# Optimization experiments

Hardware: AMD Instinct MI355X
Metric: run time of the kernel (lower is better)

## Reference

```python
import jax, jax.numpy as jnp
import numpy as np

B, T, F_IN, F_OUT, N, TP, K = 32, 12, 16, 32, 2048, 12, 3
RED = 4  # SE reduction ratio


def _conv2d(x, w, b):
    # x: [b,c,h,w_] NCHW, w: [o,i,kh,kw] OIHW, VALID padding (matches nn.Conv2d default)
    y = jax.lax.conv_general_dilated(x, w, window_strides=(1, 1), padding='VALID',
                                     dimension_numbers=('NCHW', 'OIHW', 'NCHW'))
    return y + b[None, :, None, None]


def _tconv(x, w, b, tp):
    # Tconv1: conv (1,2) -> self-pad time axis back to tp with trailing slices -> relu
    y = _conv2d(x, w, b)
    t = y.shape[-1]
    if t < tp:
        y = jnp.concatenate([y[..., -(tp - t):], y], axis=-1)
    return jax.nn.relu(y)


def setup_inputs() -> dict:
    rng = np.random.default_rng(0)
    # symmetric nonneg adjacency
    W = rng.random((N, N), dtype=np.float32)
    W = (W + W.T) * 0.5
    D = np.diag(W.sum(axis=1))
    L = (D - W).astype(np.float32)
    # lambda_max via power iteration (replaces scipy eigs 'LR')
    v = rng.standard_normal(N).astype(np.float32)
    for _ in range(100):
        v = L @ v
        v /= np.linalg.norm(v)
    lam = float(v @ (L @ v))
    Lt = (2.0 * L / lam - np.eye(N, dtype=np.float32)).astype(np.float32)
    # NOTE: original code uses ELEMENTWISE '*' (numpy) in the Chebyshev recurrence; replicate faithfully
    cheb = [np.eye(N, dtype=np.float32), Lt.copy()]
    for _ in range(2, K):
        cheb.append(2.0 * Lt * cheb[-1] - cheb[-2])
    cheb = jnp.asarray(np.stack(cheb))  # [K, N, N]

    key = jax.random.key(0)
    ks = jax.random.split(key, 16)
    s = 0.05
    hid = T // RED
    return {
        'x': jax.random.normal(ks[0], (B, T, F_IN, N), dtype=jnp.float32),
        'cheb': cheb,
        'theta1': jax.random.normal(ks[1], (K, F_IN, F_OUT), dtype=jnp.float32) * s,
        'theta2': jax.random.normal(ks[2], (K, F_OUT, F_OUT), dtype=jnp.float32) * s,
        'mlp1_w': jax.random.normal(ks[3], (hid, T), dtype=jnp.float32) * s,
        'mlp1_b': jnp.zeros((hid,), dtype=jnp.float32),
        'mlp2_w': jax.random.normal(ks[4], (T, hid), dtype=jnp.float32) * s,
        'mlp2_b': jnp.zeros((T,), dtype=jnp.float32),
        'tc1_w': jax.random.normal(ks[5], (F_OUT, F_OUT, 1, 2), dtype=jnp.float32) * s,
        'tc1_b': jnp.zeros((F_OUT,), dtype=jnp.float32),
        'tc2_w': jax.random.normal(ks[6], (F_OUT, F_OUT, 1, 2), dtype=jnp.float32) * s,
        'tc2_b': jnp.zeros((F_OUT,), dtype=jnp.float32),
        'res_w': jax.random.normal(ks[7], (F_OUT, F_IN, 1, 1), dtype=jnp.float32) * s,
        'res_b': jnp.zeros((F_OUT,), dtype=jnp.float32),
        'ln_g': jnp.ones((N,), dtype=jnp.float32),
        'ln_b': jnp.zeros((N,), dtype=jnp.float32),
    }


def reference(x, cheb, theta1, theta2, mlp1_w, mlp1_b, mlp2_w, mlp2_b,
              tc1_w, tc1_b, tc2_w, tc2_b, res_w, res_b, ln_g, ln_b):
    # --- SE channel attention over the t axis ---
    att = x.mean(axis=(2, 3))                            # [b,t] (AvgPool over full (f,n))
    att = jax.nn.relu(att @ mlp1_w.T + mlp1_b)
    att = jax.nn.sigmoid(att @ mlp2_w.T + mlp2_b)
    x_att = x * att[:, :, None, None]                    # [b,t,f,n]

    # --- Chebyshev graph conv: fused over time t and order k ---
    def gconv(h, theta):
        # original: for t, for k: (h[b,:,f,t] @ T_k) then (@ theta_k), summed over k
        z = jnp.einsum('btfm,kmn->bktfn', h, cheb)       # graph mixing, [b,K,t,f,n]
        return jnp.einsum('bktfn,kfo->bton', z, theta)   # feature mixing + k-sum -> [b,t,o,n]

    xg = jax.nn.relu(gconv(x_att, theta1))
    xg = jax.nn.relu(gconv(xg, theta2))                  # [b,t,F_OUT,n]

    # --- temporal convs ---
    xt = _tconv(xg.transpose(0, 2, 3, 1), tc1_w, tc1_b, TP)   # [b,F_OUT,n,TP]
    xt = _tconv(xt, tc2_w, tc2_b, TP).transpose(0, 3, 1, 2)   # [b,TP,F_OUT,n]

    # --- residual 1x1 conv on the original input ---
    tshort = xg.shape[1] - xt.shape[1]                   # == 0 with t == tp
    x_res = _conv2d(x[:, tshort:].transpose(0, 2, 3, 1), res_w, res_b).transpose(0, 3, 1, 2)

    y = xt + x_res                                       # [b,TP,F_OUT,n]
    # LayerNorm over last (node) axis, eps=1e-5, biased variance (torch default)
    mu = y.mean(axis=-1, keepdims=True)
    var = ((y - mu) ** 2).mean(axis=-1, keepdims=True)
    y = (y - mu) / jnp.sqrt(var + 1e-5) * ln_g + ln_b
    return jax.nn.relu(y)
```

## Files before the change

### kernel.cpp

```cpp
#include <hip/hip_runtime.h>

#define DI __device__ __forceinline__

typedef __attribute__((ext_vector_type(8))) short short8;
typedef __attribute__((ext_vector_type(4))) float f32x4;

static constexpr int Bb  = 32;
static constexpr int Tt  = 12;
static constexpr int FIN = 16;
static constexpr int NN  = 2048;
static constexpr int HID = 3;
static constexpr int M1  = Bb*Tt*FIN;
static constexpr int M2  = Bb*Tt*32;

DI float b2f(unsigned short u){
  unsigned int v = ((unsigned int)u) << 16;
  float f; __builtin_memcpy(&f, &v, 4); return f;
}
DI unsigned short f2b(float f){
  unsigned int v; __builtin_memcpy(&v, &f, 4);
  v = v + 0x7FFFu + ((v >> 16) & 1u);
  return (unsigned short)(v >> 16);
}
DI float ld(const void* p, size_t i, int flag){
  return flag ? b2f(((const unsigned short*)p)[i]) : ((const float*)p)[i];
}

typedef __attribute__((address_space(1))) const unsigned int g_u32;
typedef __attribute__((address_space(3))) unsigned int l_u32;
DI void gll16(const unsigned short* g, unsigned short* l){
  __builtin_amdgcn_global_load_lds((g_u32*)g, (l_u32*)l, 16, 0, 0);
}

__global__ void k_sniff(const unsigned short* __restrict__ x, int* __restrict__ flag,
                        float* __restrict__ att0){
  int tid = threadIdx.x;
  for (int j = tid; j < Bb*Tt; j += 64) att0[j] = 0.f;
  float v = b2f(x[tid*2]);
  int bad = (!(v == v)) || (fabsf(v) > 1e6f);
  unsigned long long m = __ballot(bad);
  if (tid == 0) *flag = (m == 0ull) ? 1 : 0;
}

__global__ void k_convert(const void* __restrict__ src, unsigned short* __restrict__ dst,
                          long long n8, const int* __restrict__ flagp, long long off,
                          float* __restrict__ att0){
  int flag = *flagp;
  int tid = threadIdx.x;
  long long i = (long long)blockIdx.x*256 + tid;
  float s = 0.f;
  if (i < n8){
    size_t base = (size_t)i * 8;
    if (flag){
      uint4 u = *(const uint4*)((const unsigned short*)src + off + base);
      *(uint4*)(dst + base) = u;
      if (att0){
        unsigned short sp[8]; __builtin_memcpy(sp, &u, 16);
        #pragma unroll
        for (int j = 0; j < 8; ++j) s += b2f(sp[j]);
      }
    } else {
      const float* f = (const float*)src + off + base;
      unsigned short o[8];
      #pragma unroll
      for (int j = 0; j < 8; ++j){ float fv = f[j]; o[j] = f2b(fv); s += fv; }
      uint4 ov; __builtin_memcpy(&ov, o, 16);
      *(uint4*)(dst + base) = ov;
    }
  }
  if (att0){
    for (int o2 = 32; o2; o2 >>= 1) s += __shfl_down(s, o2);
    __shared__ float red[4];
    if ((tid & 63) == 0) red[tid >> 6] = s;
    __syncthreads();
    if (tid == 0){
      int bt = (int)(blockIdx.x >> 4);
      atomicAdd(&att0[bt], red[0] + red[1] + red[2] + red[3]);
    }
  }
}

__global__ void k_att_mlp(const float* __restrict__ att0,
                          const void* __restrict__ m1w, const void* __restrict__ m1b,
                          const void* __restrict__ m2w, const void* __restrict__ m2b,
                          float* __restrict__ att, const int* __restrict__ flagp){
  int flag = *flagp;
  int b = threadIdx.x;
  if (b >= Bb) return;
  float a[Tt];
  #pragma unroll
  for (int t = 0; t < Tt; ++t) a[t] = att0[b*Tt + t] * (1.f / (FIN*NN));
  float h[HID];
  #pragma unroll
  for (int j = 0; j < HID; ++j){
    float s = ld(m1b, j, flag);
    #pragma unroll
    for (int t = 0; t < Tt; ++t) s += a[t] * ld(m1w, j*Tt + t, flag);
    h[j] = s > 0.f ? s : 0.f;
  }
  #pragma unroll
  for (int t = 0; t < Tt; ++t){
    float s = ld(m2b, t, flag);
    #pragma unroll
    for (int j = 0; j < HID; ++j) s += h[j] * ld(m2w, t*HID + j, flag);
    att[b*Tt + t] = 1.f / (1.f + expf(-s));
  }
}

DI void stage_tile(const unsigned short* __restrict__ Ag,
                   const unsigned short* __restrict__ chb,
                   unsigned short* Ad, unsigned short* Bd,
                   int row0, int gn0, int kk0, int tid){
  #pragma unroll
  for (int p = 0; p < 2; ++p){
    int s = tid + p*256, r = s >> 2, j = s & 3;
    gll16(Ag + (size_t)(row0 + r)*NN + kk0 + ((j ^ (r & 3)) << 3), Ad + (s << 3));
  }
  #pragma unroll
  for (int p = 0; p < 4; ++p){
    int s = tid + p*256, k = s >> 9, rem = s & 511, r = rem >> 2, j = rem & 3;
    gll16(chb + (size_t)k*NN*NN + (size_t)(gn0 + r)*NN + kk0 + ((j ^ (r & 3)) << 3), Bd + (s << 3));
  }
}

DI void compute_tile(const unsigned short* As, const unsigned short* Bs,
                     f32x4 (&acc)[2][8][2], int w, int cc, int q){
  short8 af[8];
  #pragma unroll
  for (int mt = 0; mt < 8; ++mt)
    af[mt] = *(const short8*)(As + ((mt*16 + cc) << 5) + ((q ^ (cc & 3)) << 3));
  #pragma unroll
  for (int k = 0; k < 2; ++k){
    #pragma unroll
    for (int ns = 0; ns < 2; ++ns){
      int r = w*32 + ns*16 + cc;
      short8 bv = *(const short8*)(Bs + (((k << 7) + r) << 5) + ((q ^ (cc & 3)) << 3));
      #pragma unroll
      for (int mt = 0; mt < 8; ++mt)
        acc[k][mt][ns] = __builtin_amdgcn_mfma_f32_16x16x32_bf16(af[mt], bv, acc[k][mt][ns], 0, 0, 0);
    }
  }
}

DI void wait_bar_6(){
  asm volatile("s_waitcnt vmcnt(6)" ::: "memory");
  __builtin_amdgcn_s_barrier();
  asm volatile("" ::: "memory");
}
DI void wait_bar_0(){
  asm volatile("s_waitcnt vmcnt(0)" ::: "memory");
  __builtin_amdgcn_s_barrier();
  asm volatile("" ::: "memory");
}

template <int SCALE, int F>
__global__ __launch_bounds__(256, 2)
void k_gemm(const unsigned short* __restrict__ Ag,
            const float* __restrict__ att,
            const unsigned short* __restrict__ chb,
            const void* __restrict__ theta,
            unsigned short* __restrict__ X,
            const int* __restrict__ flagp){
  constexpr int Kp = (F == 16) ? 64 : 96;
  constexpr int PP = (F == 16) ? 72 : 104;
  constexpr int G  = 128 / F;
  constexpr int NKB = Kp / 32;
  constexpr int BUF = 128*32 + 2*128*32;

  __shared__ __align__(16) unsigned short SMEM[3*BUF];
  __shared__ __align__(16) unsigned short TT[32*PP];

  int flag = *flagp;
  int tid  = threadIdx.x;
  int w    = tid >> 6, lane = tid & 63, q = lane >> 4, cc = lane & 15;
  int row0 = blockIdx.x * 128;
  int gn0  = blockIdx.y * 128;

  for (int idx = tid; idx < 32*PP; idx += 256){
    int o = idx / PP, kk = idx % PP;
    float v = (kk < 3*F) ? ld(theta, (size_t)kk*32 + o, flag) : 0.f;
    TT[idx] = f2b(v);
  }

  f32x4 zero4 = {0.f, 0.f, 0.f, 0.f};
  f32x4 acc[2][8][2];
  #pragma unroll
  for (int k = 0; k < 2; ++k)
    #pragma unroll
    for (int mt = 0; mt < 8; ++mt)
      #pragma unroll
      for (int ns = 0; ns < 2; ++ns) acc[k][mt][ns] = zero4;

  unsigned short *Ac = SMEM,           *Bc = SMEM + 4096;
  unsigned short *An = SMEM +   BUF,   *Bn = SMEM +   BUF + 4096;
  unsigned short *Af = SMEM + 2*BUF,   *Bf = SMEM + 2*BUF + 4096;

  stage_tile(Ag, chb, Ac, Bc, row0, gn0, 0,  tid);
  stage_tile(Ag, chb, An, Bn, row0, gn0, 32, tid);

  for (int it = 0; it < 63; ++it){
    wait_bar_6();
    if (it < 62) stage_tile(Ag, chb, Af, Bf, row0, gn0, (it + 2) * 32, tid);
    compute_tile(Ac, Bc, acc, w, cc, q);
    unsigned short* tA = Ac; Ac = An; An = Af; Af = tA;
    unsigned short* tB = Bc; Bc = Bn; Bn = Bf; Bf = tB;
  }
  wait_bar_0();
  compute_tile(Ac, Bc, acc, w, cc, q);

  __syncthreads();

  unsigned short* zs = SMEM + w * (32*PP);

  short8 afm[2][NKB];
  #pragma unroll
  for (int mt_o = 0; mt_o < 2; ++mt_o)
    #pragma unroll
    for (int kb = 0; kb < NKB; ++kb)
      afm[mt_o][kb] = *(const short8*)(TT + (mt_o*16 + cc)*PP + kb*32 + q*8);

  if (F == 16){
    if (lane < 32){
      #pragma unroll
      for (int j = 0; j < 4; ++j) *(uint2*)(zs + lane*PP + 48 + j*4) = make_uint2(0u, 0u);
    }
  }

  int bt0 = row0 / F;
  #pragma unroll
  for (int g = 0; g < G; ++g){
    float sc = SCALE ? att[bt0 + g] : 1.f;
    #pragma unroll
    for (int pass = 0; pass < F/16; ++pass){
      int rf = pass*16 + (lane >> 2), c8 = (lane & 3) * 8;
      uint4 u = *(const uint4*)(Ag + (size_t)(row0 + g*F + rf)*NN + gn0 + w*32 + c8);
      unsigned short sp[8]; __builtin_memcpy(sp, &u, 16);
      #pragma unroll
      for (int e = 0; e < 8; ++e){
        unsigned short val = SCALE ? f2b(b2f(sp[e]) * sc) : sp[e];
        zs[(c8 + e)*PP + rf] = val;
      }
    }
    #pragma unroll
    for (int k = 0; k < 2; ++k)
      #pragma unroll
      for (int mt_l = 0; mt_l < F/16; ++mt_l)
        #pragma unroll
        for (int ns = 0; ns < 2; ++ns){
          int mt = g*(F/16) + mt_l;
          f32x4 v = acc[k][mt][ns];
          #pragma unroll
          for (int r = 0; r < 4; ++r){
            float pv = SCALE ? v[r] * sc : v[r];
            zs[(ns*16 + cc)*PP + F*(k+1) + mt_l*16 + q*4 + r] = f2b(pv);
          }
        }
    #pragma unroll
    for (int mt_o = 0; mt_o < 2; ++mt_o)
      #pragma unroll
      for (int ch = 0; ch < 2; ++ch){
        f32x4 am = zero4;
        #pragma unroll
        for (int kb = 0; kb < NKB; ++kb){
          short8 bm = *(const short8*)(zs + (ch*16 + cc)*PP + kb*32 + q*8);
          am = __builtin_amdgcn_mfma_f32_16x16x32_bf16(afm[mt_o][kb], bm, am, 0, 0, 0);
        }
        #pragma unroll
        for (int r = 0; r < 4; ++r){
          int o = mt_o*16 + q*4 + r;
          float v = am[r]; v = v > 0.f ? v : 0.f;
          X[((size_t)((bt0 + g)*32 + o))*NN + gn0 + w*32 + ch*16 + cc] = f2b(v);
        }
      }
  }
}

__global__ void k_tconv1(const unsigned short* __restrict__ xin,
                         const void* __restrict__ wgt, const void* __restrict__ bias,
                         unsigned short* __restrict__ yout, const int* __restrict__ flagp){
  int flag = *flagp;
  __shared__ float wl[32*32*2];
  __shared__ float bl[32];
  int tid = threadIdx.x;
  for (int i = tid; i < 2048; i += 256) wl[i] = ld(wgt, i, flag);
  if (tid < 32) bl[tid] = ld(bias, tid, flag);
  __syncthreads();
  int bt = blockIdx.x, b = bt / 12, t = bt % 12;
  int c = (t == 0) ? 10 : (t - 1);
  int n = blockIdx.y*256 + tid;
  const unsigned short* p0 = xin + ((size_t)(b*12 + c  )*32)*NN + n;
  const unsigned short* p1 = xin + ((size_t)(b*12 + c+1)*32)*NN + n;
  float acc[32];
  #pragma unroll
  for (int o = 0; o < 32; ++o) acc[o] = bl[o];
  for (int i = 0; i < 32; ++i){
    float v0 = b2f(p0[(size_t)i*NN]);
    float v1 = b2f(p1[(size_t)i*NN]);
    #pragma unroll
    for (int o = 0; o < 32; ++o) acc[o] += v0*wl[o*64 + i*2] + v1*wl[o*64 + i*2 + 1];
  }
  unsigned short* op = yout + ((size_t)bt*32)*NN + n;
  #pragma unroll
  for (int o = 0; o < 32; ++o){ float v = acc[o]; op[(size_t)o*NN] = f2b(v > 0.f ? v : 0.f); }
}

__global__ __launch_bounds__(256, 2)
void k_tail(const unsigned short* __restrict__ yp,
            const void* __restrict__ x,
            const void* __restrict__ w2, const void* __restrict__ b2v,
            const void* __restrict__ rw, const void* __restrict__ rbv,
            const void* __restrict__ lng, const void* __restrict__ lnb,
            void* __restrict__ out, const int* __restrict__ flagp){
  int flag = *flagp;
  __shared__ float wt0[32*16], wt1[32*16];
  __shared__ float rt[16*16];
  __shared__ float bcv[16], rbc[16];
  __shared__ float redS[4*16], redS2[4*16];
  int tid = threadIdx.x;
  int bt = blockIdx.x, og = blockIdx.y, o0 = og*16;
  int b = bt / 12, t = bt % 12, c = (t == 0) ? 10 : (t - 1);
  for (int idx = tid; idx < 512; idx += 256){
    int i = idx >> 4, oo = idx & 15;
    wt0[idx] = ld(w2, (size_t)(o0 + oo)*64 + i*2,     flag);
    wt1[idx] = ld(w2, (size_t)(o0 + oo)*64 + i*2 + 1, flag);
  }
  if (tid < 256){
    int i = tid >> 4, oo = tid & 15;
    rt[tid] = ld(rw, (size_t)(o0 + oo)*16 + i, flag);
  }
  if (tid < 16){ bcv[tid] = ld(b2v, o0 + tid, flag); rbc[tid] = ld(rbv, o0 + tid, flag); }
  __syncthreads();
  float acc[16][8];
  #pragma unroll
  for (int oo = 0; oo < 16; ++oo)
    #pragma unroll
    for (int nn = 0; nn < 8; ++nn) acc[oo][nn] = bcv[oo];
  const unsigned short* p0 = yp + ((size_t)(b*12 + c  )*32)*NN;
  const unsigned short* p1 = yp + ((size_t)(b*12 + c+1)*32)*NN;
  for (int i = 0; i < 32; ++i){
    float v0[8], v1[8];
    #pragma unroll
    for (int nn = 0; nn < 8; ++nn){
      int n = nn*256 + tid;
      v0[nn] = b2f(p0[(size_t)i*NN + n]);
      v1[nn] = b2f(p1[(size_t)i*NN + n]);
    }
    #pragma unroll
    for (int oo = 0; oo < 16; ++oo){
      float w0 = wt0[i*16 + oo];
      float w1 = wt1[i*16 + oo];
      #pragma unroll
      for (int nn = 0; nn < 8; ++nn) acc[oo][nn] += v0[nn]*w0 + v1[nn]*w1;
    }
  }
  #pragma unroll
  for (int oo = 0; oo < 16; ++oo)
    #pragma unroll
    for (int nn = 0; nn < 8; ++nn){ float v = acc[oo][nn]; acc[oo][nn] = (v > 0.f ? v : 0.f) + rbc[oo]; }
  size_t xbase = ((size_t)(b*12 + t)*16)*NN;
  for (int i = 0; i < 16; ++i){
    float xv[8];
    #pragma unroll
    for (int nn = 0; nn < 8; ++nn) xv[nn] = ld(x, xbase + (size_t)i*NN + nn*256 + tid, flag);
    #pragma unroll
    for (int oo = 0; oo < 16; ++oo){
      float r = rt[i*16 + oo];
      #pragma unroll
      for (int nn = 0; nn < 8; ++nn) acc[oo][nn] += xv[nn]*r;
    }
  }
  int lane = tid & 63, wv = tid >> 6;
  #pragma unroll
  for (int oo = 0; oo < 16; ++oo){
    float s = 0.f, s2 = 0.f;
    #pragma unroll
    for (int nn = 0; nn < 8; ++nn){ float v = acc[oo][nn]; s += v; s2 += v*v; }
    for (int off = 32; off; off >>= 1){ s += __shfl_down(s, off); s2 += __shfl_down(s2, off); }
    if (lane == 0){ redS[wv*16 + oo] = s; redS2[wv*16 + oo] = s2; }
  }
  __syncthreads();
  size_t obase = ((size_t)((b*12 + t)*32 + o0))*NN;
  #pragma unroll
  for (int nn = 0; nn < 8; ++nn){
    int n = nn*256 + tid;
    float g = ld(lng, n, flag), be = ld(lnb, n, flag);
    #pragma unroll
    for (int oo = 0; oo < 16; ++oo){
      float S  = redS [oo] + redS [16 + oo] + redS [32 + oo] + redS [48 + oo];
      float S2 = redS2[oo] + redS2[16 + oo] + redS2[32 + oo] + redS2[48 + oo];
      float m = S * (1.f/2048.f);
      float var = S2 * (1.f/2048.f) - m*m;
      float inv = rsqrtf(var + 1e-5f);
      float v = (acc[oo][nn] - m)*inv*g + be;
      v = v > 0.f ? v : 0.f;
      if (flag) ((unsigned short*)out)[obase + (size_t)oo*NN + n] = f2b(v);
      else      ((float*)out)[obase + (size_t)oo*NN + n] = v;
    }
  }
}

extern "C" void kernel_launch(void* const* d_in, const int* in_sizes, int n_in,
                              void* d_out, int out_size, void* d_ws, size_t ws_size,
                              hipStream_t stream){
  const void* x    = d_in[0];
  const void* cheb = d_in[1];
  const void* th1  = d_in[2];
  const void* th2  = d_in[3];
  const void* m1w  = d_in[4];
  const void* m1b  = d_in[5];
  const void* m2w  = d_in[6];
  const void* m2b  = d_in[7];
  const void* t1w  = d_in[8];
  const void* t1b  = d_in[9];
  const void* t2w  = d_in[10];
  const void* t2b  = d_in[11];
  const void* rw   = d_in[12];
  const void* rb   = d_in[13];
  const void* lng  = d_in[14];
  const void* lnb  = d_in[15];
  char* ws = (char*)d_ws;

  int*   flag  = (int*)ws;
  float* att0  = (float*)(ws + 4096);
  float* att   = (float*)(ws + 8192);
  unsigned short* xb  = (unsigned short*)(ws + 16384);
  unsigned short* chb = xb + (size_t)M1*NN;
  unsigned short* X1  = chb + (size_t)2*NN*NN;
  unsigned short* X2  = (unsigned short*)d_out;
  unsigned short* Y1  = X1;

  k_sniff  <<<1, 64, 0, stream>>>((const unsigned short*)x, flag, att0);
  k_convert<<<((long long)M1*NN/8 + 255)/256, 256, 0, stream>>>(x, xb, (long long)M1*NN/8, flag, 0, att0);
  k_convert<<<((long long)2*NN*NN/8 + 255)/256, 256, 0, stream>>>(cheb, chb, (long long)2*NN*NN/8, flag, (long long)NN*NN, nullptr);
  k_att_mlp <<<1, 64, 0, stream>>>(att0, m1w, m1b, m2w, m2b, att, flag);

  k_gemm<1,16><<<dim3(M1/128, 16), 256, 0, stream>>>(xb, att, chb, th1, X1, flag);
  k_gemm<0,32><<<dim3(M2/128, 16), 256, 0, stream>>>(X1, att, chb, th2, X2, flag);

  k_tconv1<<<dim3(384, 8), 256, 0, stream>>>(X2, t1w, t1b, Y1, flag);
  k_tail  <<<dim3(384, 2), 256, 0, stream>>>(Y1, x, t2w, t2b, rw, rb, lng, lnb, d_out, flag);
}
```

Before: 778.5 us.

## Switch gconv GEMMs to double-buffered LDS and use 96-row tiles for first gconv

Replaces the triple-buffered LDS pipeline, which waited with vmcnt(6), with a two-buffer ping-pong that calls __syncthreads after each tile. The GEMM is templated on M-tile size so the first graph conv can use 96-row tiles, giving more blocks (M1/96) and better CU balance. Less LDS per block may allow higher occupancy. In exchange, the full barrier after each compute exposes load latency, because a prefetch now only overlaps one compute step.

```diff
diff --git a/kernel.cpp b/kernel.cpp
--- a/kernel.cpp
+++ b/kernel.cpp
@@ -107,14 +107,18 @@
   }
 }
 
+template <int MTILE>
 DI void stage_tile(const unsigned short* __restrict__ Ag,
                    const unsigned short* __restrict__ chb,
                    unsigned short* Ad, unsigned short* Bd,
                    int row0, int gn0, int kk0, int tid){
   #pragma unroll
   for (int p = 0; p < 2; ++p){
-    int s = tid + p*256, r = s >> 2, j = s & 3;
-    gll16(Ag + (size_t)(row0 + r)*NN + kk0 + ((j ^ (r & 3)) << 3), Ad + (s << 3));
+    int s = tid + p*256;
+    if (s < MTILE*4){
+      int r = s >> 2, j = s & 3;
+      gll16(Ag + (size_t)(row0 + r)*NN + kk0 + ((j ^ (r & 3)) << 3), Ad + (s << 3));
+    }
   }
   #pragma unroll
   for (int p = 0; p < 4; ++p){
@@ -123,11 +127,12 @@
   }
 }
 
+template <int MT>
 DI void compute_tile(const unsigned short* As, const unsigned short* Bs,
-                     f32x4 (&acc)[2][8][2], int w, int cc, int q){
-  short8 af[8];
-  #pragma unroll
-  for (int mt = 0; mt < 8; ++mt)
+                     f32x4 (&acc)[2][MT][2], int w, int cc, int q){
+  short8 af[MT];
+  #pragma unroll
+  for (int mt = 0; mt < MT; ++mt)
     af[mt] = *(const short8*)(As + ((mt*16 + cc) << 5) + ((q ^ (cc & 3)) << 3));
   #pragma unroll
   for (int k = 0; k < 2; ++k){
@@ -136,44 +141,33 @@
       int r = w*32 + ns*16 + cc;
       short8 bv = *(const short8*)(Bs + (((k << 7) + r) << 5) + ((q ^ (cc & 3)) << 3));
       #pragma unroll
-      for (int mt = 0; mt < 8; ++mt)
+      for (int mt = 0; mt < MT; ++mt)
         acc[k][mt][ns] = __builtin_amdgcn_mfma_f32_16x16x32_bf16(af[mt], bv, acc[k][mt][ns], 0, 0, 0);
     }
   }
 }
 
-DI void wait_bar_6(){
-  asm volatile("s_waitcnt vmcnt(6)" ::: "memory");
-  __builtin_amdgcn_s_barrier();
-  asm volatile("" ::: "memory");
-}
-DI void wait_bar_0(){
-  asm volatile("s_waitcnt vmcnt(0)" ::: "memory");
-  __builtin_amdgcn_s_barrier();
-  asm volatile("" ::: "memory");
-}
-
-template <int SCALE, int F>
-__global__ __launch_bounds__(256, 2)
-void k_gemm(const unsigned short* __restrict__ Ag,
-            const float* __restrict__ att,
-            const unsigned short* __restrict__ chb,
-            const void* __restrict__ theta,
-            unsigned short* __restrict__ X,
-            const int* __restrict__ flagp){
-  constexpr int Kp = (F == 16) ? 64 : 96;
-  constexpr int PP = (F == 16) ? 72 : 104;
-  constexpr int G  = 128 / F;
+template <int SCALE, int F, int MTILE>
+DI void gemm_body(const unsigned short* __restrict__ Ag,
+                  const float* __restrict__ att,
+                  const unsigned short* __restrict__ chb,
+                  const void* __restrict__ theta,
+                  unsigned short* __restrict__ X,
+                  const int* __restrict__ flagp){
+  constexpr int MT  = MTILE/16;
+  constexpr int Kp  = (F == 16) ? 64 : 96;
+  constexpr int PP  = (F == 16) ? 72 : 104;
+  constexpr int G   = MTILE / F;
   constexpr int NKB = Kp / 32;
-  constexpr int BUF = 128*32 + 2*128*32;
-
-  __shared__ __align__(16) unsigned short SMEM[3*BUF];
+  constexpr int BUF = MTILE*32 + 2*128*32;
+
+  __shared__ __align__(16) unsigned short SMEM[2*BUF];
   __shared__ __align__(16) unsigned short TT[32*PP];
 
   int flag = *flagp;
   int tid  = threadIdx.x;
   int w    = tid >> 6, lane = tid & 63, q = lane >> 4, cc = lane & 15;
-  int row0 = blockIdx.x * 128;
+  int row0 = blockIdx.x * MTILE;
   int gn0  = blockIdx.y * 128;
 
   for (int idx = tid; idx < 32*PP; idx += 256){
@@ -182,32 +176,35 @@
     TT[idx] = f2b(v);
   }
 
+  unsigned short* A0 = SMEM;
+  unsigned short* B0 = SMEM + MTILE*32;
+  unsigned short* A1 = SMEM + BUF;
+  unsigned short* B1 = SMEM + BUF + MTILE*32;
+
   f32x4 zero4 = {0.f, 0.f, 0.f, 0.f};
-  f32x4 acc[2][8][2];
+  f32x4 acc[2][MT][2];
   #pragma unroll
   for (int k = 0; k < 2; ++k)
     #pragma unroll
-    for (int mt = 0; mt < 8; ++mt)
+    for (int mt = 0; mt < MT; ++mt)
       #pragma unroll
       for (int ns = 0; ns < 2; ++ns) acc[k][mt][ns] = zero4;
 
-  unsigned short *Ac = SMEM,           *Bc = SMEM + 4096;
-  unsigned short *An = SMEM +   BUF,   *Bn = SMEM +   BUF + 4096;
-  unsigned short *Af = SMEM + 2*BUF,   *Bf = SMEM + 2*BUF + 4096;
-
-  stage_tile(Ag, chb, Ac, Bc, row0, gn0, 0,  tid);
-  stage_tile(Ag, chb, An, Bn, row0, gn0, 32, tid);
-
-  for (int it = 0; it < 63; ++it){
-    wait_bar_6();
-    if (it < 62) stage_tile(Ag, chb, Af, Bf, row0, gn0, (it + 2) * 32, tid);
-    compute_tile(Ac, Bc, acc, w, cc, q);
-    unsigned short* tA = Ac; Ac = An; An = Af; Af = tA;
-    unsigned short* tB = Bc; Bc = Bn; Bn = Bf; Bf = tB;
-  }
-  wait_bar_0();
-  compute_tile(Ac, Bc, acc, w, cc, q);
-
+  stage_tile<MTILE>(Ag, chb, A0, B0, row0, gn0, 0, tid);
+  __syncthreads();
+
+  for (int it = 0; it < 62; it += 2){
+    stage_tile<MTILE>(Ag, chb, A1, B1, row0, gn0, (it+1)*32, tid);
+    compute_tile<MT>(A0, B0, acc, w, cc, q);
+    __syncthreads();
+    stage_tile<MTILE>(Ag, chb, A0, B0, row0, gn0, (it+2)*32, tid);
+    compute_tile<MT>(A1, B1, acc, w, cc, q);
+    __syncthreads();
+  }
+  stage_tile<MTILE>(Ag, chb, A1, B1, row0, gn0, 63*32, tid);
+  compute_tile<MT>(A0, B0, acc, w, cc, q);
+  __syncthreads();
+  compute_tile<MT>(A1, B1, acc, w, cc, q);
   __syncthreads();
 
   unsigned short* zs = SMEM + w * (32*PP);
@@ -273,6 +270,19 @@
         }
       }
   }
+}
+
+__global__ __launch_bounds__(256, 2)
+void k_gconv1(const unsigned short* __restrict__ Ag, const float* __restrict__ att,
+              const unsigned short* __restrict__ chb, const void* __restrict__ theta,
+              unsigned short* __restrict__ X, const int* __restrict__ flagp){
+  gemm_body<1, 16, 96>(Ag, att, chb, theta, X, flagp);
+}
+__global__ __launch_bounds__(256, 2)
+void k_gconv2(const unsigned short* __restrict__ Ag, const float* __restrict__ att,
+              const unsigned short* __restrict__ chb, const void* __restrict__ theta,
+              unsigned short* __restrict__ X, const int* __restrict__ flagp){
+  gemm_body<0, 32, 128>(Ag, att, chb, theta, X, flagp);
 }
 
 __global__ void k_tconv1(const unsigned short* __restrict__ xin,
@@ -434,8 +444,8 @@
   k_convert<<<((long long)2*NN*NN/8 + 255)/256, 256, 0, stream>>>(cheb, chb, (long long)2*NN*NN/8, flag, (long long)NN*NN, nullptr);
   k_att_mlp <<<1, 64, 0, stream>>>(att0, m1w, m1b, m2w, m2b, att, flag);
 
-  k_gemm<1,16><<<dim3(M1/128, 16), 256, 0, stream>>>(xb, att, chb, th1, X1, flag);
-  k_gemm<0,32><<<dim3(M2/128, 16), 256, 0, stream>>>(X1, att, chb, th2, X2, flag);
+  k_gconv1<<<dim3(M1/96, 16), 256, 0, stream>>>(xb, att, chb, th1, X1, flag);
+  k_gconv2<<<dim3(M2/128, 16), 256, 0, stream>>>(X1, att, chb, th2, X2, flag);
 
   k_tconv1<<<dim3(384, 8), 256, 0, stream>>>(X2, t1w, t1b, Y1, flag);
   k_tail  <<<dim3(384, 2), 256, 0, stream>>>(Y1, x, t2w, t2b, rw, rb, lng, lnb, d_out, flag);
```

Measured after the change: 742.0 us. -4.7%, faster.
